# Kernel tuning notes

Hardware: AMD Instinct MI355X
Metric: run time of the kernel (lower is better)

## Reference

```python
import jax, jax.numpy as jnp
import numpy as np
import math

J = 32            # output capsules (init j)
N = 16            # capsule dim (init n)
MASK_PERCENT = [0.4, 0.4]  # sparse top-k fractions per routing update


def squash(s, eps=1e-8):
    # v = (|s|^2 / (1+|s|^2)) * s/|s|
    sq = jnp.sum(s * s, axis=-1, keepdims=True)
    return (sq / (1.0 + sq)) * (s / jnp.sqrt(sq + eps))


def calc_entropy(c, axis):
    # -sum c*log(c), with 0*log0 := 0 (masked-out capsules have c == 0)
    safe = jnp.where(c > 0, c, 1.0)
    return -jnp.sum(jnp.where(c > 0, c * jnp.log(safe), 0.0), axis=axis)


def _sparsify_topk(b_vec, it, i):
    # method='topk', target='nodes': keep top select_count output capsules per example
    select_count = J
    for prev in MASK_PERCENT[: it + 1]:
        select_count = math.ceil(select_count * (1 - prev))
    if select_count >= J:
        return b_vec
    c = jax.nn.softmax(b_vec, axis=1)            # (b, j, i)
    scores = c.sum(axis=2) / i                   # (b, j) node scores
    _, idx = jax.lax.top_k(scores, select_count) # (b, k)
    b = scores.shape[0]
    sel = jnp.zeros((b, J), bool).at[jnp.arange(b)[:, None], idx].set(True)
    return jnp.where(sel[:, :, None], b_vec, -jnp.inf)


def setup_inputs() -> dict:
    key = jax.random.key(0)
    b, i = 128, 1152
    u_hat = jax.random.normal(key, (b, J, i, N), dtype=jnp.float32)
    bias = jnp.full((J, N), 0.1, dtype=jnp.float32)  # b_routing init 0.1
    return {"u_hat": u_hat, "bias": bias, "iters": 3}


def reference(u_hat, bias, iters):
    b, j, i, n = u_hat.shape
    b_vec = jnp.zeros((b, j, i), u_hat.dtype)
    entropies = []
    v_vec = None
    for index in range(iters):
        c_vec = jax.nn.softmax(b_vec, axis=1)                  # softmax over j
        entropies.append(calc_entropy(c_vec, axis=1).mean(axis=1))  # (b,)
        s_vec = jnp.einsum('bji,bjin->bjn', c_vec, u_hat)      # (b, j, n)
        reset_mask = jnp.sum(s_vec, axis=2) == 0               # (b, j)
        s_vec_bias = jnp.where(reset_mask[..., None], 0.0, s_vec + bias)
        v_vec = squash(s_vec_bias)                             # (b, j, n)
        if index < iters - 1:
            b_vec = b_vec + jnp.einsum('bjin,bjn->bji', u_hat, v_vec)
            b_vec = _sparsify_topk(b_vec, index, i)
    entropy_layer = jnp.stack(entropies, axis=1)               # (b, iters)
    return v_vec, entropy_layer
```

## Files before the change

kernel.cpp:

```cpp
#include <hip/hip_runtime.h>
#include <math.h>

#define B_ 128
#define J_ 32
#define I_ 1152
#define N_ 16
#define TI 16
#define STEPS 4
#define NT (I_/(TI*STEPS))

#define OFF_W   0
#define OFF_S1  65536
#define OFF_S2  131072
#define OFF_S0  196608
#define OFF_SC0 262144
#define OFF_SC1 266240
#define OFF_M0  270336
#define OFF_M1  274432

__global__ void zero_kernel(float* __restrict__ ws, float* __restrict__ ent) {
    int idx = blockIdx.x * 256 + threadIdx.x;
    const int n = 2 * 65536 + 2 * 4096;
    for (int k = idx; k < n; k += gridDim.x * 256) ws[OFF_S1 + k] = 0.f;
    if (idx < B_ * 3) ent[idx] = 0.f;
}

__global__ void sum_kernel(const float* __restrict__ U, float* __restrict__ s0) {
    int bj  = blockIdx.x;
    int tid = threadIdx.x;
    int nc  = tid & 3;
    int ip  = tid >> 2;
    const float4* base = (const float4*)(U + (size_t)bj * I_ * N_);
    float4 acc = make_float4(0.f, 0.f, 0.f, 0.f);
    for (int i = ip; i < I_; i += 64) {
        float4 u = base[i * 4 + nc];
        acc.x += u.x; acc.y += u.y; acc.z += u.z; acc.w += u.w;
    }
    __shared__ float4 lds[256];
    lds[nc * 64 + ip] = acc;
    __syncthreads();
    for (int s = 32; s >= 1; s >>= 1) {
        if (ip < s) {
            float4 a = lds[nc * 64 + ip], b = lds[nc * 64 + ip + s];
            a.x += b.x; a.y += b.y; a.z += b.z; a.w += b.w;
            lds[nc * 64 + ip] = a;
        }
        __syncthreads();
    }
    if (ip == 0) ((float4*)s0)[bj * 4 + nc] = lds[nc * 64];
}

__global__ void vupdate_kernel(const float* __restrict__ s, const float* __restrict__ bias,
                               float* __restrict__ w, float* __restrict__ out_v,
                               float* __restrict__ ent, float scale, int mode) {
    int b = blockIdx.x;
    int tid = threadIdx.x;
    int j = tid >> 4, n = tid & 15;
    int idx = (b * J_ + j) * N_ + n;
    float sv = s[idx] * scale;
    float rs = sv;
    for (int k = 8; k; k >>= 1) rs += __shfl_xor(rs, k);
    float sb = (rs == 0.f) ? 0.f : sv + bias[j * N_ + n];
    float sq = sb * sb;
    for (int k = 8; k; k >>= 1) sq += __shfl_xor(sq, k);
    float v = (sq / (1.f + sq)) * (sb / sqrtf(sq + 1e-8f));
    if (mode == 0) {
        w[idx] = v;
        if (tid == 0) ent[b * 3] = logf(32.f);
    } else if (mode == 1) {
        w[idx] += v;
    } else {
        out_v[idx] = v;
    }
}

__global__ __launch_bounds__(256) void pass_kernel(
        const float* __restrict__ U, const float* __restrict__ w,
        const int* __restrict__ mask, float* __restrict__ scores,
        float* __restrict__ s_out, float* __restrict__ ent,
        int ent_idx, int mode, int rev) {
    __shared__ float4 lds[J_ * (TI * 4 + 1)];
    __shared__ float le[256];

    int bid = rev ? (gridDim.x - 1 - blockIdx.x) : blockIdx.x;
    int b = bid / NT, chunk = bid % NT;
    int i0 = chunk * (TI * STEPS);
    int tid = threadIdx.x;
    int j = tid & 31, sub = tid >> 5;

    const float4* wp = (const float4*)(w + (b * J_ + j) * N_);
    float4 w0 = wp[0], w1 = wp[1], w2 = wp[2], w3 = wp[3];
    bool active = mask ? (mask[b * J_ + j] != 0) : true;

    float acc_sc = 0.f, acc_ent = 0.f;
    float4 a0 = make_float4(0,0,0,0), a1 = a0, a2 = a0, a3 = a0;

    const float4* Ub = (const float4*)U;

    for (int st = 0; st < STEPS; ++st) {
        int ibase = i0 + st * TI;
        #pragma unroll
        for (int r = 0; r < 8; ++r) {
            int f  = tid + 256 * r;
            int js = f >> 6;
            int q  = f & 63;
            lds[js * 65 + q] = Ub[((size_t)(b * J_ + js) * I_ + ibase) * 4 + q];
        }
        __syncthreads();
        #pragma unroll
        for (int t2 = 0; t2 < 2; ++t2) {
            int ii = sub + t2 * 8;
            const float4* up = &lds[j * 65 + ii * 4];
            float4 u0 = up[0], u1 = up[1], u2 = up[2], u3 = up[3];
            float y = u0.x * w0.x + u0.y * w0.y + u0.z * w0.z + u0.w * w0.w
                    + u1.x * w1.x + u1.y * w1.y + u1.z * w1.z + u1.w * w1.w
                    + u2.x * w2.x + u2.y * w2.y + u2.z * w2.z + u2.w * w2.w
                    + u3.x * w3.x + u3.y * w3.y + u3.z * w3.z + u3.w * w3.w;
            float e = active ? __expf(y) : 0.f;
            float Z = e;
            for (int k = 16; k; k >>= 1) Z += __shfl_xor(Z, k);
            float p = e / Z;
            if (mode == 0) {
                acc_sc += p;
            } else {
                a0.x += p * u0.x; a0.y += p * u0.y; a0.z += p * u0.z; a0.w += p * u0.w;
                a1.x += p * u1.x; a1.y += p * u1.y; a1.z += p * u1.z; a1.w += p * u1.w;
                a2.x += p * u2.x; a2.y += p * u2.y; a2.z += p * u2.z; a2.w += p * u2.w;
                a3.x += p * u3.x; a3.y += p * u3.y; a3.z += p * u3.z; a3.w += p * u3.w;
                acc_ent += p * (y - __logf(Z));
            }
        }
        __syncthreads();
    }

    if (mode == 0) {
        le[tid] = acc_sc;
        __syncthreads();
        if (tid < 32) {
            float t = 0.f;
            for (int s = 0; s < 8; s++) t += le[s * 32 + tid];
            atomicAdd(&scores[b * J_ + tid], t);
        }
    } else {
        float* ls = (float*)lds;
        float* myl = ls + tid * 16;
        ((float4*)myl)[0] = a0; ((float4*)myl)[1] = a1;
        ((float4*)myl)[2] = a2; ((float4*)myl)[3] = a3;
        le[tid] = acc_ent;
        __syncthreads();
        for (int idx = tid; idx < 512; idx += 256) {
            int jj = idx >> 4, nn = idx & 15;
            float t = 0.f;
            for (int s = 0; s < 8; s++) t += ls[(s * 32 + jj) * 16 + nn];
            atomicAdd(&s_out[(b * J_ + jj) * N_ + nn], t);
        }
        for (int s = 128; s >= 1; s >>= 1) {
            if (tid < s) le[tid] += le[tid + s];
            __syncthreads();
        }
        if (tid == 0) atomicAdd(&ent[b * 3 + ent_idx], -le[0] * (1.f / (float)I_));
    }
}

__global__ void topk_kernel(const float* __restrict__ scores, int* __restrict__ mask, int K) {
    int b = blockIdx.x;
    int tid = threadIdx.x;
    __shared__ float ls[32];
    if (tid < 32) ls[tid] = scores[b * 32 + tid];
    __syncthreads();
    if (tid < 32) {
        float sv = ls[tid];
        int rank = 0;
        for (int jj = 0; jj < 32; jj++) {
            float o = ls[jj];
            rank += (o > sv) || (o == sv && jj < tid);
        }
        mask[b * 32 + tid] = (rank < K) ? 1 : 0;
    }
}

extern "C" void kernel_launch(void* const* d_in, const int* in_sizes, int n_in,
                              void* d_out, int out_size, void* d_ws, size_t ws_size,
                              hipStream_t stream) {
    const float* U    = (const float*)d_in[0];
    const float* bias = (const float*)d_in[1];
    float* ws  = (float*)d_ws;
    float* out = (float*)d_out;
    float* ent = out + B_ * J_ * N_;

    float* w   = ws + OFF_W;
    float* s0  = ws + OFF_S0;
    float* s1  = ws + OFF_S1;
    float* s2  = ws + OFF_S2;
    float* sc0 = ws + OFF_SC0;
    float* sc1 = ws + OFF_SC1;
    int*   m0  = (int*)(ws + OFF_M0);
    int*   m1  = (int*)(ws + OFF_M1);

    zero_kernel<<<544, 256, 0, stream>>>(ws, ent);

    sum_kernel<<<B_ * J_, 256, 0, stream>>>(U, s0);
    vupdate_kernel<<<B_, 512, 0, stream>>>(s0, bias, w, nullptr, ent, 1.f / 32.f, 0);

    pass_kernel<<<B_ * NT, 256, 0, stream>>>(U, w, nullptr, sc0, nullptr, nullptr, 0, 0, 1);
    topk_kernel<<<B_, 64, 0, stream>>>(sc0, m0, 20);

    pass_kernel<<<B_ * NT, 256, 0, stream>>>(U, w, m0, nullptr, s1, ent, 1, 1, 0);
    vupdate_kernel<<<B_, 512, 0, stream>>>(s1, bias, w, nullptr, ent, 1.f, 1);

    pass_kernel<<<B_ * NT, 256, 0, stream>>>(U, w, m0, sc1, nullptr, nullptr, 0, 0, 1);
    topk_kernel<<<B_, 64, 0, stream>>>(sc1, m1, 12);

    pass_kernel<<<B_ * NT, 256, 0, stream>>>(U, w, m1, nullptr, s2, ent, 2, 1, 0);
    vupdate_kernel<<<B_, 512, 0, stream>>>(s2, bias, nullptr, out, ent, 1.f, 2);
}
```

Before: 603.6 us.

## Transpose u_hat once to (b,i,j,n) and stream passes directly from global

A new first kernel transposes u_hat into a workspace copy laid out as (b, i, j, n) and computes the initial per-capsule sums at the same time, using atomics for the sums. The four routing passes then read that copy directly with coalesced loads and register prefetch, so they no longer stage through LDS or need barriers. The cost is an extra 75 MB write plus a read of the transposed copy. The block-order reversal trick that aimed for L2 reuse between passes is also removed.

```diff
diff --git a/kernel.cpp b/kernel.cpp
--- a/kernel.cpp
+++ b/kernel.cpp
@@ -5,9 +5,6 @@
 #define J_ 32
 #define I_ 1152
 #define N_ 16
-#define TI 16
-#define STEPS 4
-#define NT (I_/(TI*STEPS))
 
 #define OFF_W   0
 #define OFF_S1  65536
@@ -17,37 +14,60 @@
 #define OFF_SC1 266240
 #define OFF_M0  270336
 #define OFF_M1  274432
+#define OFF_UT  524288
+
+#define TCH 32
+#define TNB (I_/TCH)
+#define RS  520
+
+#define PCH 64
+#define PNB (I_/PCH)
 
 __global__ void zero_kernel(float* __restrict__ ws, float* __restrict__ ent) {
     int idx = blockIdx.x * 256 + threadIdx.x;
-    const int n = 2 * 65536 + 2 * 4096;
+    const int n = 3 * 65536 + 2 * 4096;
     for (int k = idx; k < n; k += gridDim.x * 256) ws[OFF_S1 + k] = 0.f;
     if (idx < B_ * 3) ent[idx] = 0.f;
 }
 
-__global__ void sum_kernel(const float* __restrict__ U, float* __restrict__ s0) {
-    int bj  = blockIdx.x;
-    int tid = threadIdx.x;
-    int nc  = tid & 3;
-    int ip  = tid >> 2;
-    const float4* base = (const float4*)(U + (size_t)bj * I_ * N_);
-    float4 acc = make_float4(0.f, 0.f, 0.f, 0.f);
-    for (int i = ip; i < I_; i += 64) {
-        float4 u = base[i * 4 + nc];
-        acc.x += u.x; acc.y += u.y; acc.z += u.z; acc.w += u.w;
-    }
-    __shared__ float4 lds[256];
-    lds[nc * 64 + ip] = acc;
+__global__ __launch_bounds__(256) void transpose_sum_kernel(
+        const float* __restrict__ U, float* __restrict__ Ut, float* __restrict__ s0) {
+    __shared__ float lds[TCH * RS];
+    int bid = blockIdx.x;
+    int b = bid / TNB, chunk = bid % TNB;
+    int i0 = chunk * TCH;
+    int tid = threadIdx.x;
+    int w = tid >> 6, l = tid & 63;
+    const float4* U4 = (const float4*)U;
+    float4* Ut4 = (float4*)Ut;
+
+    for (int jj = 0; jj < 8; ++jj) {
+        int j = w * 8 + jj;
+        const float4* pb = U4 + ((size_t)(b * J_ + j) * I_ + i0) * 4;
+        float4 d0 = pb[l];
+        float4 d1 = pb[l + 64];
+        int il = l >> 2, c = l & 3;
+        *(float4*)&lds[il * RS + j * 16 + c * 4]        = d0;
+        *(float4*)&lds[(il + 16) * RS + j * 16 + c * 4] = d1;
+        float4 a = make_float4(d0.x + d1.x, d0.y + d1.y, d0.z + d1.z, d0.w + d1.w);
+        for (int k = 4; k <= 32; k <<= 1) {
+            a.x += __shfl_xor(a.x, k); a.y += __shfl_xor(a.y, k);
+            a.z += __shfl_xor(a.z, k); a.w += __shfl_xor(a.w, k);
+        }
+        if (l < 4) {
+            float* sp = s0 + (b * J_ + j) * N_ + l * 4;
+            atomicAdd(sp + 0, a.x); atomicAdd(sp + 1, a.y);
+            atomicAdd(sp + 2, a.z); atomicAdd(sp + 3, a.w);
+        }
+    }
     __syncthreads();
-    for (int s = 32; s >= 1; s >>= 1) {
-        if (ip < s) {
-            float4 a = lds[nc * 64 + ip], b = lds[nc * 64 + ip + s];
-            a.x += b.x; a.y += b.y; a.z += b.z; a.w += b.w;
-            lds[nc * 64 + ip] = a;
-        }
-        __syncthreads();
-    }
-    if (ip == 0) ((float4*)s0)[bj * 4 + nc] = lds[nc * 64];
+    float4* ob = Ut4 + (size_t)(b * I_ + i0) * (J_ * 4);
+    #pragma unroll
+    for (int k = 0; k < 16; ++k) {
+        int f = tid + 256 * k;
+        int il = f >> 7, q = f & 127;
+        ob[f] = *(const float4*)&lds[il * RS + q * 4];
+    }
 }
 
 __global__ void vupdate_kernel(const float* __restrict__ s, const float* __restrict__ bias,
@@ -75,18 +95,18 @@
 }
 
 __global__ __launch_bounds__(256) void pass_kernel(
-        const float* __restrict__ U, const float* __restrict__ w,
+        const float* __restrict__ Ut, const float* __restrict__ w,
         const int* __restrict__ mask, float* __restrict__ scores,
         float* __restrict__ s_out, float* __restrict__ ent,
-        int ent_idx, int mode, int rev) {
-    __shared__ float4 lds[J_ * (TI * 4 + 1)];
+        int ent_idx, int mode) {
+    __shared__ float ls[4096];
     __shared__ float le[256];
 
-    int bid = rev ? (gridDim.x - 1 - blockIdx.x) : blockIdx.x;
-    int b = bid / NT, chunk = bid % NT;
-    int i0 = chunk * (TI * STEPS);
-    int tid = threadIdx.x;
-    int j = tid & 31, sub = tid >> 5;
+    int bid = blockIdx.x;
+    int b = bid / PNB, chunk = bid % PNB;
+    int i0 = chunk * PCH;
+    int tid = threadIdx.x;
+    int j = tid & 31, ig = tid >> 5;
 
     const float4* wp = (const float4*)(w + (b * J_ + j) * N_);
     float4 w0 = wp[0], w1 = wp[1], w2 = wp[2], w3 = wp[3];
@@ -95,42 +115,36 @@
     float acc_sc = 0.f, acc_ent = 0.f;
     float4 a0 = make_float4(0,0,0,0), a1 = a0, a2 = a0, a3 = a0;
 
-    const float4* Ub = (const float4*)U;
-
-    for (int st = 0; st < STEPS; ++st) {
-        int ibase = i0 + st * TI;
-        #pragma unroll
-        for (int r = 0; r < 8; ++r) {
-            int f  = tid + 256 * r;
-            int js = f >> 6;
-            int q  = f & 63;
-            lds[js * 65 + q] = Ub[((size_t)(b * J_ + js) * I_ + ibase) * 4 + q];
-        }
-        __syncthreads();
-        #pragma unroll
-        for (int t2 = 0; t2 < 2; ++t2) {
-            int ii = sub + t2 * 8;
-            const float4* up = &lds[j * 65 + ii * 4];
-            float4 u0 = up[0], u1 = up[1], u2 = up[2], u3 = up[3];
-            float y = u0.x * w0.x + u0.y * w0.y + u0.z * w0.z + u0.w * w0.w
-                    + u1.x * w1.x + u1.y * w1.y + u1.z * w1.z + u1.w * w1.w
-                    + u2.x * w2.x + u2.y * w2.y + u2.z * w2.z + u2.w * w2.w
-                    + u3.x * w3.x + u3.y * w3.y + u3.z * w3.z + u3.w * w3.w;
-            float e = active ? __expf(y) : 0.f;
-            float Z = e;
-            for (int k = 16; k; k >>= 1) Z += __shfl_xor(Z, k);
-            float p = e / Z;
-            if (mode == 0) {
-                acc_sc += p;
-            } else {
-                a0.x += p * u0.x; a0.y += p * u0.y; a0.z += p * u0.z; a0.w += p * u0.w;
-                a1.x += p * u1.x; a1.y += p * u1.y; a1.z += p * u1.z; a1.w += p * u1.w;
-                a2.x += p * u2.x; a2.y += p * u2.y; a2.z += p * u2.z; a2.w += p * u2.w;
-                a3.x += p * u3.x; a3.y += p * u3.y; a3.z += p * u3.z; a3.w += p * u3.w;
-                acc_ent += p * (y - __logf(Z));
-            }
-        }
-        __syncthreads();
+    const float4* Ut4 = (const float4*)Ut;
+    size_t idx4 = ((size_t)(b * I_ + i0 + ig) * J_ + j) * 4;
+    const size_t stp = (size_t)8 * J_ * 4;
+
+    float4 u0 = Ut4[idx4], u1 = Ut4[idx4 + 1], u2 = Ut4[idx4 + 2], u3 = Ut4[idx4 + 3];
+    #pragma unroll
+    for (int t = 0; t < 8; ++t) {
+        float4 n0 = u0, n1 = u1, n2 = u2, n3 = u3;
+        if (t < 7) {
+            idx4 += stp;
+            n0 = Ut4[idx4]; n1 = Ut4[idx4 + 1]; n2 = Ut4[idx4 + 2]; n3 = Ut4[idx4 + 3];
+        }
+        float y = u0.x * w0.x + u0.y * w0.y + u0.z * w0.z + u0.w * w0.w
+                + u1.x * w1.x + u1.y * w1.y + u1.z * w1.z + u1.w * w1.w
+                + u2.x * w2.x + u2.y * w2.y + u2.z * w2.z + u2.w * w2.w
+                + u3.x * w3.x + u3.y * w3.y + u3.z * w3.z + u3.w * w3.w;
+        float e = active ? __expf(y) : 0.f;
+        float Z = e;
+        for (int k = 16; k; k >>= 1) Z += __shfl_xor(Z, k);
+        float p = e / Z;
+        if (mode == 0) {
+            acc_sc += p;
+        } else {
+            a0.x += p * u0.x; a0.y += p * u0.y; a0.z += p * u0.z; a0.w += p * u0.w;
+            a1.x += p * u1.x; a1.y += p * u1.y; a1.z += p * u1.z; a1.w += p * u1.w;
+            a2.x += p * u2.x; a2.y += p * u2.y; a2.z += p * u2.z; a2.w += p * u2.w;
+            a3.x += p * u3.x; a3.y += p * u3.y; a3.z += p * u3.z; a3.w += p * u3.w;
+            acc_ent += p * (y - __logf(Z));
+        }
+        u0 = n0; u1 = n1; u2 = n2; u3 = n3;
     }
 
     if (mode == 0) {
@@ -142,7 +156,6 @@
             atomicAdd(&scores[b * J_ + tid], t);
         }
     } else {
-        float* ls = (float*)lds;
         float* myl = ls + tid * 16;
         ((float4*)myl)[0] = a0; ((float4*)myl)[1] = a1;
         ((float4*)myl)[2] = a2; ((float4*)myl)[3] = a3;
@@ -196,21 +209,22 @@
     float* sc1 = ws + OFF_SC1;
     int*   m0  = (int*)(ws + OFF_M0);
     int*   m1  = (int*)(ws + OFF_M1);
+    float* Ut  = ws + OFF_UT;
 
     zero_kernel<<<544, 256, 0, stream>>>(ws, ent);
 
-    sum_kernel<<<B_ * J_, 256, 0, stream>>>(U, s0);
+    transpose_sum_kernel<<<B_ * TNB, 256, 0, stream>>>(U, Ut, s0);
     vupdate_kernel<<<B_, 512, 0, stream>>>(s0, bias, w, nullptr, ent, 1.f / 32.f, 0);
 
-    pass_kernel<<<B_ * NT, 256, 0, stream>>>(U, w, nullptr, sc0, nullptr, nullptr, 0, 0, 1);
+    pass_kernel<<<B_ * PNB, 256, 0, stream>>>(Ut, w, nullptr, sc0, nullptr, nullptr, 0, 0);
     topk_kernel<<<B_, 64, 0, stream>>>(sc0, m0, 20);
 
-    pass_kernel<<<B_ * NT, 256, 0, stream>>>(U, w, m0, nullptr, s1, ent, 1, 1, 0);
+    pass_kernel<<<B_ * PNB, 256, 0, stream>>>(Ut, w, m0, nullptr, s1, ent, 1, 1);
     vupdate_kernel<<<B_, 512, 0, stream>>>(s1, bias, w, nullptr, ent, 1.f, 1);
 
-    pass_kernel<<<B_ * NT, 256, 0, stream>>>(U, w, m0, sc1, nullptr, nullptr, 0, 0, 1);
+    pass_kernel<<<B_ * PNB, 256, 0, stream>>>(Ut, w, m0, sc1, nullptr, nullptr, 0, 0);
     topk_kernel<<<B_, 64, 0, stream>>>(sc1, m1, 12);
 
-    pass_kernel<<<B_ * NT, 256, 0, stream>>>(U, w, m1, nullptr, s2, ent, 2, 1, 0);
+    pass_kernel<<<B_ * PNB, 256, 0, stream>>>(Ut, w, m1, nullptr, s2, ent, 2, 1);
     vupdate_kernel<<<B_, 512, 0, stream>>>(s2, bias, nullptr, out, ent, 1.f, 2);
 }
```

Result: slower. 670.2 us (+11.0%).
